# Kernel tuning notes

Measured on AMD Instinct MI355X. Metric: run time of the kernel, lower is better.

## Reference

```python
import jax, jax.numpy as jnp
import numpy as np

THETA = 10000.0


def apply_rope(x, token_position, theta=THETA):
    # x: [B, H, S, d_k] with interleaved even/odd pairs; token_position: [B, S]
    B, H, S, d_k = x.shape
    inv_freq = 1.0 / theta ** (jnp.arange(0, d_k, 2, dtype=jnp.float32) / d_k)  # [d_k/2]
    angles = token_position.astype(jnp.float32)[:, :, None] * inv_freq[None, None, :]  # [B,S,d_k/2]
    cos = jnp.cos(angles)[:, None, :, :]  # [B,1,S,d_k/2]
    sin = jnp.sin(angles)[:, None, :, :]
    xp = x.reshape(B, H, S, d_k // 2, 2)
    x_even, x_odd = xp[..., 0], xp[..., 1]
    rot_even = x_even * cos - x_odd * sin
    rot_odd = x_even * sin + x_odd * cos
    return jnp.stack([rot_even, rot_odd], axis=-1).reshape(B, H, S, d_k)


def setup_inputs() -> dict:
    key = jax.random.key(0)
    ks = jax.random.split(key, 6)
    B, S, D = 2, 2048, 2048
    x = jax.random.normal(ks[0], (B, S, D), dtype=jnp.float32)
    token_position = jnp.sort(jax.random.randint(ks[1], (B, S), 0, 2048), axis=-1).astype(jnp.int32)
    scale = 0.02
    WQ = jax.random.normal(ks[2], (D, D), dtype=jnp.float32) * scale
    WK = jax.random.normal(ks[3], (D, D), dtype=jnp.float32) * scale
    WV = jax.random.normal(ks[4], (D, D), dtype=jnp.float32) * scale
    WO = jax.random.normal(ks[5], (D, D), dtype=jnp.float32) * scale
    return {"x": x, "token_position": token_position, "WQ": WQ, "WK": WK, "WV": WV, "WO": WO}


def reference(x, token_position, WQ, WK, WV, WO):
    B, S, D = x.shape
    H = 16
    d_k = D // H

    def proj(W):
        return jnp.matmul(x, W).reshape(B, S, H, d_k).transpose(0, 2, 1, 3)  # [B,H,S,d_k]

    Q = apply_rope(proj(WQ), token_position)
    K = apply_rope(proj(WK), token_position)
    V = proj(WV)

    score = jnp.einsum('bhqd,bhkd->bhqk', Q, K) / jnp.sqrt(jnp.float32(d_k))
    causal = jnp.triu(jnp.full((S, S), -jnp.inf, dtype=jnp.float32), k=1)
    score = score + causal
    attn = jax.nn.softmax(score, axis=-1)  # stable max-sub softmax, same math
    out = jnp.einsum('bhqk,bhkd->bhqd', attn, V)
    out = out.transpose(0, 2, 1, 3).reshape(B, S, D)
    return jnp.matmul(out, WO)
```

## Files before the change

kernel.cpp:

```cpp
#include <hip/hip_runtime.h>
#include <hip/hip_bf16.h>
#include <cstdint>
#include <cstddef>

typedef unsigned short u16;
typedef __attribute__((ext_vector_type(4))) unsigned short u16x4;
typedef __attribute__((ext_vector_type(8))) unsigned short u16x8;
typedef __attribute__((ext_vector_type(8))) __bf16 bf16x8;
typedef __attribute__((ext_vector_type(4))) float f32x4;

#define MFMA16(a, b, c) __builtin_amdgcn_mfma_f32_16x16x32_bf16((a), (b), (c), 0, 0, 0)

__device__ __forceinline__ u16 f2bf(float f) {
  uint32_t u = __builtin_bit_cast(uint32_t, f);
  u += 0x7FFFu + ((u >> 16) & 1u);
  return (u16)(u >> 16);
}
__device__ __forceinline__ float bf2f(u16 h) {
  return __builtin_bit_cast(float, (uint32_t)h << 16);
}

typedef const __attribute__((address_space(1))) void gv_t;
typedef __attribute__((address_space(3))) void lv_t;
__device__ __forceinline__ void gload16(const void* g, void* l) {
  __builtin_amdgcn_global_load_lds((gv_t*)g, (lv_t*)l, 16, 0, 0);
}

__global__ void prep(const float* __restrict__ x, const float* __restrict__ w0,
                     const float* __restrict__ w1, const float* __restrict__ w2,
                     const float* __restrict__ w3, u16* __restrict__ xb,
                     u16* __restrict__ wtbase) {
  const int z = blockIdx.z;
  const int bx = blockIdx.x, by = blockIdx.y;
  const int tx = threadIdx.x, ty = threadIdx.y;
  if (z >= 4) {
    const int i = ((z - 4) * 4096 + by * 64 + bx) * 256 + ty * 32 + tx;
    float4 v = ((const float4*)x)[i];
    u16x4 o;
    o[0] = f2bf(v.x); o[1] = f2bf(v.y); o[2] = f2bf(v.z); o[3] = f2bf(v.w);
    ((u16x4*)xb)[i] = o;
    return;
  }
  __shared__ float tile[32][33];
  const float* in = (z == 0) ? w0 : (z == 1) ? w1 : (z == 2) ? w2 : w3;
  u16* out = wtbase + (size_t)z * 4194304;
#pragma unroll
  for (int i = 0; i < 32; i += 8)
    tile[ty + i][tx] = in[(size_t)(by * 32 + ty + i) * 2048 + bx * 32 + tx];
  __syncthreads();
#pragma unroll
  for (int i = 0; i < 32; i += 8)
    out[(size_t)(bx * 32 + ty + i) * 2048 + by * 32 + tx] = f2bf(tile[tx][ty + i]);
}

template <int MODE>
__global__ __launch_bounds__(512, 1) void gemm8(const u16* __restrict__ A,
                                                const u16* __restrict__ Bt,
                                                void* __restrict__ Cv,
                                                const int* __restrict__ pos, int nbn) {
  constexpr int K = 2048;
  __shared__ __align__(16) u16 lds[73728];
  const int tid = threadIdx.x, lane = tid & 63;
  const int lo16 = lane & 15, hi = lane >> 4;
  const int wid = tid >> 6;
  const int wr = wid >> 1, wc = wid & 1;

  const int xcd = (int)blockIdx.x & 7;
  const int idx = (int)blockIdx.x >> 3;
  const int cpx = nbn >> 3;
  const int bn = (xcd * cpx + idx % cpx) * 128;
  const int bm = (idx / cpx) * 256;

  const int srow = tid >> 3;
  const int scol = ((tid & 7) ^ (srow & 7)) * 8;
  const u16* Arow = A + (size_t)(bm + srow) * K + scol;
  const u16* Brow = Bt + (size_t)(bn + srow) * K + scol;
  char* dstbase = (char*)lds + tid * 16;

#define STG_A(qb_, t_, r_) \
  gload16(Arow + (size_t)(r_) * 64 * K + (t_) * 64, dstbase + (qb_) * 49152 + (r_) * 8192)
#define STG_B(qb_, t_, r_) \
  gload16(Brow + (size_t)(r_) * 64 * K + (t_) * 64, dstbase + (qb_) * 49152 + 32768 + (r_) * 8192)

  f32x4 acc[4][4];
  const f32x4 z4 = {0.f, 0.f, 0.f, 0.f};
#pragma unroll
  for (int m = 0; m < 4; ++m)
#pragma unroll
    for (int n = 0; n < 4; ++n) acc[m][n] = z4;

  const int xork = lo16 & 7;
  const int aRow = (wr * 64 + lo16) * 128;
  const int bRow = 32768 + (wc * 64 + lo16) * 128;
  const int x0 = ((hi ^ xork)) << 4;
  const int x1 = (((4 + hi) ^ xork)) << 4;

  STG_A(0, 0, 0); STG_A(0, 0, 1); STG_B(0, 0, 0); STG_A(0, 0, 2); STG_A(0, 0, 3); STG_B(0, 0, 1);
  STG_A(1, 1, 0); STG_A(1, 1, 1); STG_B(1, 1, 0); STG_A(1, 1, 2); STG_A(1, 1, 3); STG_B(1, 1, 1);

  int q = 0;
  for (int t = 0; t < 32; ++t) {
    if (t < 31) {
      asm volatile("s_waitcnt vmcnt(6)" ::: "memory");
    } else {
      asm volatile("s_waitcnt vmcnt(0)" ::: "memory");
    }
    __builtin_amdgcn_s_barrier();
    __builtin_amdgcn_sched_barrier(0);
    const char* Aq = (const char*)lds + q * 49152;
    const int q2 = (q == 0) ? 2 : q - 1;

    bf16x8 b0[4], b1[4], a0[2], a1[2];
#pragma unroll
    for (int n = 0; n < 4; ++n) b0[n] = *(const bf16x8*)(Aq + bRow + n * 2048 + x0);
#pragma unroll
    for (int n = 0; n < 4; ++n) b1[n] = *(const bf16x8*)(Aq + bRow + n * 2048 + x1);
#pragma unroll
    for (int m = 0; m < 2; ++m) a0[m] = *(const bf16x8*)(Aq + aRow + m * 2048 + x0);
#pragma unroll
    for (int m = 0; m < 2; ++m) a1[m] = *(const bf16x8*)(Aq + aRow + m * 2048 + x1);
    if (t < 30) { STG_A(q2, t + 2, 0); STG_A(q2, t + 2, 1); STG_B(q2, t + 2, 0); }
    __builtin_amdgcn_sched_barrier(0);
    __builtin_amdgcn_s_setprio(1);
#pragma unroll
    for (int m = 0; m < 2; ++m)
#pragma unroll
      for (int n = 0; n < 4; ++n) acc[m][n] = MFMA16(a0[m], b0[n], acc[m][n]);
#pragma unroll
    for (int m = 0; m < 2; ++m)
#pragma unroll
      for (int n = 0; n < 4; ++n) acc[m][n] = MFMA16(a1[m], b1[n], acc[m][n]);
    __builtin_amdgcn_s_setprio(0);

    bf16x8 c0[2], c1[2];
#pragma unroll
    for (int m = 0; m < 2; ++m) c0[m] = *(const bf16x8*)(Aq + aRow + (m + 2) * 2048 + x0);
#pragma unroll
    for (int m = 0; m < 2; ++m) c1[m] = *(const bf16x8*)(Aq + aRow + (m + 2) * 2048 + x1);
    if (t < 30) { STG_A(q2, t + 2, 2); STG_A(q2, t + 2, 3); STG_B(q2, t + 2, 1); }
    __builtin_amdgcn_sched_barrier(0);
    __builtin_amdgcn_s_barrier();
    __builtin_amdgcn_sched_barrier(0);
    __builtin_amdgcn_s_setprio(1);
#pragma unroll
    for (int m = 0; m < 2; ++m)
#pragma unroll
      for (int n = 0; n < 4; ++n) acc[m + 2][n] = MFMA16(c0[m], b0[n], acc[m + 2][n]);
#pragma unroll
    for (int m = 0; m < 2; ++m)
#pragma unroll
      for (int n = 0; n < 4; ++n) acc[m + 2][n] = MFMA16(c1[m], b1[n], acc[m + 2][n]);
    __builtin_amdgcn_s_setprio(0);
    q = (q == 2) ? 0 : q + 1;
  }
#undef STG_A
#undef STG_B

  if constexpr (MODE == 2) {
    const int sect = bn >> 11;
    u16* Cq = (u16*)Cv + (size_t)sect * 8388608;
    const int cb = (bn & 2047) + wc * 64;
    if (sect < 2) {
      const float qsc = (sect == 0) ? 0.08838834764831845f : 1.0f;
      float freq[4];
#pragma unroll
      for (int n = 0; n < 4; ++n) {
        const int c = cb + n * 16 + lo16;
        freq[n] = exp2f((float)((c & 127) >> 1) * -0.2076205059304601f);
      }
      const float sg = (lo16 & 1) ? 1.f : -1.f;
#pragma unroll
      for (int m = 0; m < 4; ++m) {
        const int row = bm + wr * 64 + m * 16 + hi * 4;
#pragma unroll
        for (int r = 0; r < 4; ++r) {
          const float p = (float)pos[row + r];
#pragma unroll
          for (int n = 0; n < 4; ++n) {
            const float ang = p * freq[n];
            const float sn = __sinf(ang);
            const float cs = __cosf(ang);
            const float v = acc[m][n][r];
            const float pv = __shfl_xor(v, 1);
            Cq[(size_t)(row + r) * 2048 + cb + n * 16 + lo16] =
                f2bf((v * cs + sg * pv * sn) * qsc);
          }
        }
      }
    } else {
      __syncthreads();
#pragma unroll
      for (int m = 0; m < 4; ++m) {
#pragma unroll
        for (int n = 0; n < 4; ++n) {
          const int d = wc * 64 + n * 16 + lo16;
          const int tokb = wr * 64 + m * 16 + hi * 4;
#pragma unroll
          for (int r = 0; r < 4; ++r)
            lds[d * 260 + tokb + r] = f2bf(acc[m][n][r]);
        }
      }
      __syncthreads();
      const int b = bm >> 11, hh = (bn & 2047) >> 7;
      u16* vt = Cq + ((size_t)((b * 16 + hh) * 128)) * 2048 + (bm & 2047);
#pragma unroll
      for (int j = 0; j < 4; ++j) {
        const int d = (tid >> 4) + j * 32;
        const int t0 = (tid & 15) * 16;
        const u16* src = lds + d * 260 + t0;
        u16* dst = vt + (size_t)d * 2048 + t0;
#pragma unroll
        for (int w = 0; w < 4; ++w)
          *(u16x4*)(dst + w * 4) = *(const u16x4*)(src + w * 4);
      }
    }
  } else {
    float* C = (float*)Cv;
    const int cb = bn + wc * 64;
#pragma unroll
    for (int m = 0; m < 4; ++m)
#pragma unroll
      for (int n = 0; n < 4; ++n)
#pragma unroll
        for (int r = 0; r < 4; ++r)
          C[(size_t)(bm + wr * 64 + m * 16 + hi * 4 + r) * 2048 + cb + n * 16 + lo16] =
              acc[m][n][r];
  }
}

__global__ __launch_bounds__(256, 2) void flash_attn4(const u16* __restrict__ Qb,
                                                      const u16* __restrict__ Kb,
                                                      const u16* __restrict__ VT,
                                                      u16* __restrict__ Ob) {
  constexpr int S = 2048, HD = 2048;
  const int g = (int)blockIdx.x;
  const int xcd = g & 7, slot = g >> 3;
  const int bh = xcd * 4 + (slot & 3);
  const int pairid = slot >> 2;
  const int b = bh >> 4, h = bh & 15;
  const int tid = threadIdx.x, lane = tid & 63, wid = tid >> 6;

  __shared__ u16 Ks[2][64 * 128];
  __shared__ u16 Vs[2][128 * 64];
  __shared__ u16 Ps[4][16 * 64];

  const size_t base = (size_t)b * S * HD + (size_t)h * 128;
  const u16* Qp = Qb + base;
  const u16* Kp = Kb + base;
  const u16* VTp = VT + (size_t)bh * 128 * S;
  u16* Op = Ob + base;

  const f32x4 z4 = {0.f, 0.f, 0.f, 0.f};
  const int kKv = (lane >> 4);
  const int kC16 = (lane & 15);
  const int vD = (lane >> 3);
  const int vC16 = (lane & 7);

#define STAGE(pb, kv0_)                                                                   \
  {                                                                                       \
    _Pragma("unroll") for (int c = 0; c < 4; ++c) {                                       \
      const int ch = wid * 4 + c;                                                         \
      {                                                                                   \
        const int kv = ch * 4 + kKv;                                                      \
        const int c16 = kC16 ^ (kv & 7);                                                  \
        gload16(Kp + (size_t)((kv0_) + kv) * HD + c16 * 8, (char*)Ks[pb] + ch * 1024);    \
      }                                                                                   \
      {                                                                                   \
        const int d = ch * 8 + vD;                                                        \
        const int c16 = vC16 ^ (d & 7);                                                   \
        gload16(VTp + (size_t)d * S + (kv0_) + c16 * 8, (char*)Vs[pb] + ch * 1024);       \
      }                                                                                   \
    }                                                                                     \
  }

#pragma unroll
  for (int half = 0; half < 2; ++half) {
    const int qt = half ? pairid : 31 - pairid;
    const int q0 = qt * 64;

    bf16x8 qf[4];
    {
      const int qr = q0 + wid * 16 + (lane & 15);
      const int kc = (lane >> 4) * 8;
#pragma unroll
      for (int kb = 0; kb < 4; ++kb)
        qf[kb] = *(const bf16x8*)(Qp + (size_t)qr * HD + kb * 32 + kc);
    }

    f32x4 accO[8];
#pragma unroll
    for (int d = 0; d < 8; ++d) accO[d] = z4;
    float m_r[4] = {-INFINITY, -INFINITY, -INFINITY, -INFINITY};
    float l_r[4] = {0.f, 0.f, 0.f, 0.f};

    STAGE(0, 0);

    for (int t = 0; t <= qt; ++t) {
      const int cur = t & 1;
      const int kv0 = t * 64;
      if (t < qt) {
        STAGE(cur ^ 1, kv0 + 64);
        asm volatile("s_waitcnt vmcnt(8)" ::: "memory");
      } else {
        asm volatile("s_waitcnt vmcnt(0)" ::: "memory");
      }
      __builtin_amdgcn_s_barrier();
      __builtin_amdgcn_sched_barrier(0);

      const u16* Ksc = Ks[cur];
      const u16* Vsc = Vs[cur];
      f32x4 accS[4];
#pragma unroll
      for (int nb = 0; nb < 4; ++nb) accS[nb] = z4;

      __builtin_amdgcn_s_setprio(1);
#pragma unroll
      for (int nb = 0; nb < 4; ++nb) {
        const int kv = nb * 16 + (lane & 15);
#pragma unroll
        for (int kb = 0; kb < 4; ++kb) {
          const int c16 = (kb * 4 + (lane >> 4)) ^ (kv & 7);
          bf16x8 kf = *(const bf16x8*)((char*)Ksc + kv * 256 + c16 * 16);
          accS[nb] = MFMA16(qf[kb], kf, accS[nb]);
        }
      }
      __builtin_amdgcn_s_setprio(0);

      if (t == qt) {
#pragma unroll
        for (int nb = 0; nb < 4; ++nb) {
          const int kv = kv0 + nb * 16 + (lane & 15);
          const int qrow = q0 + wid * 16 + (lane >> 4) * 4;
#pragma unroll
          for (int j = 0; j < 4; ++j)
            if (kv > qrow + j) accS[nb][j] = -INFINITY;
        }
      }

      float lm[4];
#pragma unroll
      for (int j = 0; j < 4; ++j)
        lm[j] = fmaxf(fmaxf(accS[0][j], accS[1][j]), fmaxf(accS[2][j], accS[3][j]));
      const bool ok = (lm[0] <= m_r[0] + 8.f) && (lm[1] <= m_r[1] + 8.f) &&
                      (lm[2] <= m_r[2] + 8.f) && (lm[3] <= m_r[3] + 8.f);
      if (!__all(ok)) {
#pragma unroll
        for (int j = 0; j < 4; ++j) {
          float mx = lm[j];
#pragma unroll
          for (int off = 1; off < 16; off <<= 1) mx = fmaxf(mx, __shfl_xor(mx, off));
          const float mn = fmaxf(m_r[j], mx);
          const float sc = __expf(m_r[j] - mn);
          m_r[j] = mn;
          l_r[j] *= sc;
#pragma unroll
          for (int db = 0; db < 8; ++db) accO[db][j] *= sc;
        }
      }

      u16* Pw = &Ps[wid][0];
#pragma unroll
      for (int j = 0; j < 4; ++j) {
        float s = 0.f;
#pragma unroll
        for (int nb = 0; nb < 4; ++nb) {
          const float p = __expf(accS[nb][j] - m_r[j]);
          accS[nb][j] = p;
          s += p;
        }
        l_r[j] += s;
        const int ql = (lane >> 4) * 4 + j;
#pragma unroll
        for (int nb = 0; nb < 4; ++nb) {
          const int col = nb * 16 + (lane & 15);
          const int byteoff = ql * 128 + ((((col >> 3) ^ (ql & 7))) << 4) + (col & 7) * 2;
          *(u16*)((char*)Pw + byteoff) = f2bf(accS[nb][j]);
        }
      }

#pragma unroll
      for (int kb2 = 0; kb2 < 2; ++kb2) {
        const int ql = lane & 15;
        const int c16a = (kb2 * 4 + (lane >> 4)) ^ (ql & 7);
        bf16x8 pa = *(const bf16x8*)((char*)Pw + ql * 128 + c16a * 16);
        __builtin_amdgcn_s_setprio(1);
#pragma unroll
        for (int db = 0; db < 8; ++db) {
          const int d = db * 16 + (lane & 15);
          const int c16 = (kb2 * 4 + (lane >> 4)) ^ (d & 7);
          bf16x8 vf = *(const bf16x8*)((char*)Vsc + d * 128 + c16 * 16);
          accO[db] = MFMA16(pa, vf, accO[db]);
        }
        __builtin_amdgcn_s_setprio(0);
      }
      __builtin_amdgcn_sched_barrier(0);
      __builtin_amdgcn_s_barrier();
    }

    float inv[4];
#pragma unroll
    for (int j = 0; j < 4; ++j) {
      float l = l_r[j];
#pragma unroll
      for (int off = 1; off < 16; off <<= 1) l += __shfl_xor(l, off);
      inv[j] = 1.f / l;
    }
#pragma unroll
    for (int db = 0; db < 8; ++db)
#pragma unroll
      for (int j = 0; j < 4; ++j) {
        const int row = q0 + wid * 16 + (lane >> 4) * 4 + j;
        Op[(size_t)row * HD + db * 16 + (lane & 15)] = f2bf(accO[db][j] * inv[j]);
      }
  }
#undef STAGE
}

extern "C" void kernel_launch(void* const* d_in, const int* in_sizes, int n_in,
                              void* d_out, int out_size, void* d_ws, size_t ws_size,
                              hipStream_t stream) {
  const float* x  = (const float*)d_in[0];
  const int*   tp = (const int*)d_in[1];
  const float* WQ = (const float*)d_in[2];
  const float* WK = (const float*)d_in[3];
  const float* WV = (const float*)d_in[4];
  const float* WO = (const float*)d_in[5];

  const size_t MB = 1024 * 1024;
  if (ws_size < 112 * MB) return;
  char* ws = (char*)d_ws;
  u16* xb  = (u16*)(ws + 0 * MB);
  u16* wqt = (u16*)(ws + 16 * MB);
  u16* wot = (u16*)(ws + 40 * MB);
  u16* Qb  = (u16*)(ws + 48 * MB);
  u16* Kb  = (u16*)(ws + 64 * MB);
  u16* VTb = (u16*)(ws + 80 * MB);
  u16* Obf = (u16*)(ws + 96 * MB);

  {
    dim3 g(64, 64, 6), blk(32, 8);
    prep<<<g, blk, 0, stream>>>(x, WQ, WK, WV, WO, xb, wqt);
  }
  gemm8<2><<<768, 512, 0, stream>>>(xb, wqt, (void*)Qb, tp, 48);

  flash_attn4<<<512, 256, 0, stream>>>(Qb, Kb, VTb, Obf);

  gemm8<1><<<256, 512, 0, stream>>>(Obf, wot, d_out, nullptr, 16);
}
```

Baseline: 236.4 us.

## Process both paired query tiles in one KV sweep to share K/V loads

Each block handled two causal query tiles (a long one and a short one) one after the other, staging K/V twice. Now both tiles are processed together in a single pass over KV, and each staged K/V tile is reused for both. This removes the second staging pass and its global loads and barriers. The cost is roughly doubled Q-fragment and accumulator registers, which may cause spills or lower occupancy under launch_bounds(256,2), and the shared P buffer is now used sequentially by both steps.

```diff
diff --git a/kernel.cpp b/kernel.cpp
--- a/kernel.cpp
+++ b/kernel.cpp
@@ -228,7 +228,96 @@
   }
 }
 
-__global__ __launch_bounds__(256, 2) void flash_attn4(const u16* __restrict__ Qb,
+__device__ __forceinline__ void attn_step(const char* Ksc, const char* Vsc, char* Pw,
+                                          const bf16x8* qf, f32x4* accO,
+                                          float* m_r, float* l_r,
+                                          bool diag, int kv0, int qrow0, int lane) {
+  const f32x4 z4 = {0.f, 0.f, 0.f, 0.f};
+  f32x4 accS[4];
+#pragma unroll
+  for (int nb = 0; nb < 4; ++nb) accS[nb] = z4;
+
+  __builtin_amdgcn_s_setprio(1);
+#pragma unroll
+  for (int nb = 0; nb < 4; ++nb) {
+    const int kv = nb * 16 + (lane & 15);
+#pragma unroll
+    for (int kb = 0; kb < 4; ++kb) {
+      const int c16 = (kb * 4 + (lane >> 4)) ^ (kv & 7);
+      bf16x8 kf = *(const bf16x8*)(Ksc + kv * 256 + c16 * 16);
+      accS[nb] = MFMA16(qf[kb], kf, accS[nb]);
+    }
+  }
+  __builtin_amdgcn_s_setprio(0);
+
+  if (diag) {
+#pragma unroll
+    for (int nb = 0; nb < 4; ++nb) {
+      const int kv = kv0 + nb * 16 + (lane & 15);
+#pragma unroll
+      for (int j = 0; j < 4; ++j)
+        if (kv > qrow0 + j) accS[nb][j] = -INFINITY;
+    }
+  }
+
+  float lm[4];
+#pragma unroll
+  for (int j = 0; j < 4; ++j)
+    lm[j] = fmaxf(fmaxf(accS[0][j], accS[1][j]), fmaxf(accS[2][j], accS[3][j]));
+  const bool ok = (lm[0] <= m_r[0] + 8.f) && (lm[1] <= m_r[1] + 8.f) &&
+                  (lm[2] <= m_r[2] + 8.f) && (lm[3] <= m_r[3] + 8.f);
+  if (!__all(ok)) {
+#pragma unroll
+    for (int j = 0; j < 4; ++j) {
+      float mx = lm[j];
+#pragma unroll
+      for (int off = 1; off < 16; off <<= 1) mx = fmaxf(mx, __shfl_xor(mx, off));
+      const float mn = fmaxf(m_r[j], mx);
+      const float sc = __expf(m_r[j] - mn);
+      m_r[j] = mn;
+      l_r[j] *= sc;
+#pragma unroll
+      for (int db = 0; db < 8; ++db) accO[db][j] *= sc;
+    }
+  }
+
+#pragma unroll
+  for (int j = 0; j < 4; ++j) {
+    float s = 0.f;
+#pragma unroll
+    for (int nb = 0; nb < 4; ++nb) {
+      const float p = __expf(accS[nb][j] - m_r[j]);
+      accS[nb][j] = p;
+      s += p;
+    }
+    l_r[j] += s;
+    const int ql = (lane >> 4) * 4 + j;
+#pragma unroll
+    for (int nb = 0; nb < 4; ++nb) {
+      const int col = nb * 16 + (lane & 15);
+      const int byteoff = ql * 128 + ((((col >> 3) ^ (ql & 7))) << 4) + (col & 7) * 2;
+      *(u16*)(Pw + byteoff) = f2bf(accS[nb][j]);
+    }
+  }
+
+#pragma unroll
+  for (int kb2 = 0; kb2 < 2; ++kb2) {
+    const int ql = lane & 15;
+    const int c16a = (kb2 * 4 + (lane >> 4)) ^ (ql & 7);
+    bf16x8 pa = *(const bf16x8*)(Pw + ql * 128 + c16a * 16);
+    __builtin_amdgcn_s_setprio(1);
+#pragma unroll
+    for (int db = 0; db < 8; ++db) {
+      const int d = db * 16 + (lane & 15);
+      const int c16 = (kb2 * 4 + (lane >> 4)) ^ (d & 7);
+      bf16x8 vf = *(const bf16x8*)(Vsc + d * 128 + c16 * 16);
+      accO[db] = MFMA16(pa, vf, accO[db]);
+    }
+    __builtin_amdgcn_s_setprio(0);
+  }
+}
+
+__global__ __launch_bounds__(256, 2) void flash_attn8(const u16* __restrict__ Qb,
                                                       const u16* __restrict__ Kb,
                                                       const u16* __restrict__ VT,
                                                       u16* __restrict__ Ob) {
@@ -239,6 +328,8 @@
   const int pairid = slot >> 2;
   const int b = bh >> 4, h = bh & 15;
   const int tid = threadIdx.x, lane = tid & 63, wid = tid >> 6;
+  const int qtA = 31 - pairid, qtB = pairid;
+  const int q0a = qtA * 64, q0b = qtB * 64;
 
   __shared__ u16 Ks[2][64 * 128];
   __shared__ u16 Vs[2][128 * 64];
@@ -273,147 +364,78 @@
     }                                                                                     \
   }
 
-#pragma unroll
-  for (int half = 0; half < 2; ++half) {
-    const int qt = half ? pairid : 31 - pairid;
-    const int q0 = qt * 64;
-
-    bf16x8 qf[4];
-    {
-      const int qr = q0 + wid * 16 + (lane & 15);
-      const int kc = (lane >> 4) * 8;
-#pragma unroll
-      for (int kb = 0; kb < 4; ++kb)
-        qf[kb] = *(const bf16x8*)(Qp + (size_t)qr * HD + kb * 32 + kc);
-    }
-
-    f32x4 accO[8];
-#pragma unroll
-    for (int d = 0; d < 8; ++d) accO[d] = z4;
-    float m_r[4] = {-INFINITY, -INFINITY, -INFINITY, -INFINITY};
-    float l_r[4] = {0.f, 0.f, 0.f, 0.f};
-
-    STAGE(0, 0);
-
-    for (int t = 0; t <= qt; ++t) {
-      const int cur = t & 1;
-      const int kv0 = t * 64;
-      if (t < qt) {
-        STAGE(cur ^ 1, kv0 + 64);
-        asm volatile("s_waitcnt vmcnt(8)" ::: "memory");
-      } else {
-        asm volatile("s_waitcnt vmcnt(0)" ::: "memory");
-      }
-      __builtin_amdgcn_s_barrier();
-      __builtin_amdgcn_sched_barrier(0);
-
-      const u16* Ksc = Ks[cur];
-      const u16* Vsc = Vs[cur];
-      f32x4 accS[4];
-#pragma unroll
-      for (int nb = 0; nb < 4; ++nb) accS[nb] = z4;
-
-      __builtin_amdgcn_s_setprio(1);
-#pragma unroll
-      for (int nb = 0; nb < 4; ++nb) {
-        const int kv = nb * 16 + (lane & 15);
-#pragma unroll
-        for (int kb = 0; kb < 4; ++kb) {
-          const int c16 = (kb * 4 + (lane >> 4)) ^ (kv & 7);
-          bf16x8 kf = *(const bf16x8*)((char*)Ksc + kv * 256 + c16 * 16);
-          accS[nb] = MFMA16(qf[kb], kf, accS[nb]);
-        }
-      }
-      __builtin_amdgcn_s_setprio(0);
-
-      if (t == qt) {
-#pragma unroll
-        for (int nb = 0; nb < 4; ++nb) {
-          const int kv = kv0 + nb * 16 + (lane & 15);
-          const int qrow = q0 + wid * 16 + (lane >> 4) * 4;
-#pragma unroll
-          for (int j = 0; j < 4; ++j)
-            if (kv > qrow + j) accS[nb][j] = -INFINITY;
-        }
-      }
-
-      float lm[4];
-#pragma unroll
-      for (int j = 0; j < 4; ++j)
-        lm[j] = fmaxf(fmaxf(accS[0][j], accS[1][j]), fmaxf(accS[2][j], accS[3][j]));
-      const bool ok = (lm[0] <= m_r[0] + 8.f) && (lm[1] <= m_r[1] + 8.f) &&
-                      (lm[2] <= m_r[2] + 8.f) && (lm[3] <= m_r[3] + 8.f);
-      if (!__all(ok)) {
-#pragma unroll
-        for (int j = 0; j < 4; ++j) {
-          float mx = lm[j];
-#pragma unroll
-          for (int off = 1; off < 16; off <<= 1) mx = fmaxf(mx, __shfl_xor(mx, off));
-          const float mn = fmaxf(m_r[j], mx);
-          const float sc = __expf(m_r[j] - mn);
-          m_r[j] = mn;
-          l_r[j] *= sc;
-#pragma unroll
-          for (int db = 0; db < 8; ++db) accO[db][j] *= sc;
-        }
-      }
-
-      u16* Pw = &Ps[wid][0];
-#pragma unroll
-      for (int j = 0; j < 4; ++j) {
-        float s = 0.f;
-#pragma unroll
-        for (int nb = 0; nb < 4; ++nb) {
-          const float p = __expf(accS[nb][j] - m_r[j]);
-          accS[nb][j] = p;
-          s += p;
-        }
-        l_r[j] += s;
-        const int ql = (lane >> 4) * 4 + j;
-#pragma unroll
-        for (int nb = 0; nb < 4; ++nb) {
-          const int col = nb * 16 + (lane & 15);
-          const int byteoff = ql * 128 + ((((col >> 3) ^ (ql & 7))) << 4) + (col & 7) * 2;
-          *(u16*)((char*)Pw + byteoff) = f2bf(accS[nb][j]);
-        }
-      }
-
-#pragma unroll
-      for (int kb2 = 0; kb2 < 2; ++kb2) {
-        const int ql = lane & 15;
-        const int c16a = (kb2 * 4 + (lane >> 4)) ^ (ql & 7);
-        bf16x8 pa = *(const bf16x8*)((char*)Pw + ql * 128 + c16a * 16);
-        __builtin_amdgcn_s_setprio(1);
-#pragma unroll
-        for (int db = 0; db < 8; ++db) {
-          const int d = db * 16 + (lane & 15);
-          const int c16 = (kb2 * 4 + (lane >> 4)) ^ (d & 7);
-          bf16x8 vf = *(const bf16x8*)((char*)Vsc + d * 128 + c16 * 16);
-          accO[db] = MFMA16(pa, vf, accO[db]);
-        }
-        __builtin_amdgcn_s_setprio(0);
-      }
-      __builtin_amdgcn_sched_barrier(0);
-      __builtin_amdgcn_s_barrier();
-    }
-
-    float inv[4];
+  bf16x8 qfA[4], qfB[4];
+  {
+    const int kc = (lane >> 4) * 8;
+    const int qrA = q0a + wid * 16 + (lane & 15);
+    const int qrB = q0b + wid * 16 + (lane & 15);
+#pragma unroll
+    for (int kb = 0; kb < 4; ++kb) {
+      qfA[kb] = *(const bf16x8*)(Qp + (size_t)qrA * HD + kb * 32 + kc);
+      qfB[kb] = *(const bf16x8*)(Qp + (size_t)qrB * HD + kb * 32 + kc);
+    }
+  }
+
+  f32x4 accOA[8], accOB[8];
+#pragma unroll
+  for (int d = 0; d < 8; ++d) { accOA[d] = z4; accOB[d] = z4; }
+  float mA[4] = {-INFINITY, -INFINITY, -INFINITY, -INFINITY};
+  float lA[4] = {0.f, 0.f, 0.f, 0.f};
+  float mB[4] = {-INFINITY, -INFINITY, -INFINITY, -INFINITY};
+  float lB[4] = {0.f, 0.f, 0.f, 0.f};
+
+  const int qrow0A = q0a + wid * 16 + (lane >> 4) * 4;
+  const int qrow0B = q0b + wid * 16 + (lane >> 4) * 4;
+  char* Pw = (char*)&Ps[wid][0];
+
+  STAGE(0, 0);
+
+  for (int t = 0; t <= qtA; ++t) {
+    const int cur = t & 1;
+    const int kv0 = t * 64;
+    if (t < qtA) {
+      STAGE(cur ^ 1, kv0 + 64);
+      asm volatile("s_waitcnt vmcnt(8)" ::: "memory");
+    } else {
+      asm volatile("s_waitcnt vmcnt(0)" ::: "memory");
+    }
+    __builtin_amdgcn_s_barrier();
+    __builtin_amdgcn_sched_barrier(0);
+
+    const char* Ksc = (const char*)Ks[cur];
+    const char* Vsc = (const char*)Vs[cur];
+
+    attn_step(Ksc, Vsc, Pw, qfA, accOA, mA, lA, t == qtA, kv0, qrow0A, lane);
+
+    if (t <= qtB)
+      attn_step(Ksc, Vsc, Pw, qfB, accOB, mB, lB, t == qtB, kv0, qrow0B, lane);
+
+    __builtin_amdgcn_sched_barrier(0);
+    __builtin_amdgcn_s_barrier();
+  }
+#undef STAGE
+
+  float invA[4], invB[4];
+#pragma unroll
+  for (int j = 0; j < 4; ++j) {
+    float la = lA[j], lb = lB[j];
+#pragma unroll
+    for (int off = 1; off < 16; off <<= 1) {
+      la += __shfl_xor(la, off);
+      lb += __shfl_xor(lb, off);
+    }
+    invA[j] = 1.f / la;
+    invB[j] = 1.f / lb;
+  }
+#pragma unroll
+  for (int db = 0; db < 8; ++db)
 #pragma unroll
     for (int j = 0; j < 4; ++j) {
-      float l = l_r[j];
-#pragma unroll
-      for (int off = 1; off < 16; off <<= 1) l += __shfl_xor(l, off);
-      inv[j] = 1.f / l;
-    }
-#pragma unroll
-    for (int db = 0; db < 8; ++db)
-#pragma unroll
-      for (int j = 0; j < 4; ++j) {
-        const int row = q0 + wid * 16 + (lane >> 4) * 4 + j;
-        Op[(size_t)row * HD + db * 16 + (lane & 15)] = f2bf(accO[db][j] * inv[j]);
-      }
-  }
-#undef STAGE
+      const int rowA = qrow0A + j;
+      const int rowB = qrow0B + j;
+      Op[(size_t)rowA * HD + db * 16 + (lane & 15)] = f2bf(accOA[db][j] * invA[j]);
+      Op[(size_t)rowB * HD + db * 16 + (lane & 15)] = f2bf(accOB[db][j] * invB[j]);
+    }
 }
 
 extern "C" void kernel_launch(void* const* d_in, const int* in_sizes, int n_in,
@@ -443,7 +465,7 @@
   }
   gemm8<2><<<768, 512, 0, stream>>>(xb, wqt, (void*)Qb, tp, 48);
 
-  flash_attn4<<<512, 256, 0, stream>>>(Qb, Kb, VTb, Obf);
+  flash_attn8<<<512, 256, 0, stream>>>(Qb, Kb, VTb, Obf);
 
   gemm8<1><<<256, 512, 0, stream>>>(Obf, wot, d_out, nullptr, 16);
 }
```

After: 236.1 us. No clear change (-0.1%).
